# Kernel optimization log

Measured on AMD Instinct MI355X. Metric: run time of the kernel, lower is better.

## Reference

```python
import jax, jax.numpy as jnp
import numpy as np

TEMPERATURE = 0.2
EPS = 1e-10

def setup_inputs() -> dict:
    key = jax.random.key(0)
    x = jax.random.normal(key, (8, 1024, 64, 64), dtype=jnp.float32)
    return {"x": x}

def reference(x):
    B, C, H, W = x.shape
    xf = x.reshape(B, C, H * W)                      # [B, C, HW]
    dot = jnp.einsum('bcn,bdn->bcd', xf, xf) / TEMPERATURE  # [B, C, C]
    logits = jax.nn.softmax(dot, axis=-1)
    diag = jnp.diagonal(logits, axis1=-2, axis2=-1)  # [B, C]
    loss = -jnp.log(diag + EPS)
    return jnp.mean(loss)
```

## Files before the change

kernel.cpp:

```cpp
#include <hip/hip_runtime.h>
#include <hip/hip_bf16.h>

#define BATCH 8
#define CCH 1024
#define NHW 4096
#define SCALE 5.0f
#define ROWS (BATCH * CCH)
#define NTILES 72
#define NTICK (BATCH * NTILES)
#define GRID_G 512

typedef unsigned char u8;
typedef unsigned int u32;
typedef __attribute__((ext_vector_type(4))) float float4v;
typedef __attribute__((ext_vector_type(4))) u32 uint4v;

__device__ __forceinline__ void async_load16(const void* gsrc, void* ldst) {
    __builtin_amdgcn_global_load_lds(
        (__attribute__((address_space(1))) void*)gsrc,
        (__attribute__((address_space(3))) void*)ldst,
        16, 0, 0);
}

__device__ __forceinline__ u32 pk4_fp8(float a, float b, float c, float d) {
    u32 v = __builtin_amdgcn_cvt_pk_fp8_f32(a, b, 0, false);
    v = __builtin_amdgcn_cvt_pk_fp8_f32(c, d, v, true);
    return v;
}

__device__ __forceinline__ float ssq4_fp8(u32 q) {
    float d0 = __builtin_amdgcn_cvt_f32_fp8(q, 0);
    float d1 = __builtin_amdgcn_cvt_f32_fp8(q, 1);
    float d2 = __builtin_amdgcn_cvt_f32_fp8(q, 2);
    float d3 = __builtin_amdgcn_cvt_f32_fp8(q, 3);
    return d0 * d0 + d1 * d1 + d2 * d2 + d3 * d3;
}

template <bool CONVERT>
__global__ __launch_bounds__(256) void prep_kernel(const float* __restrict__ x,
                                                   u8* __restrict__ xq,
                                                   float* __restrict__ diag,
                                                   float* __restrict__ l_acc,
                                                   int* __restrict__ counters) {
    const int row = blockIdx.x;
    const int tid = threadIdx.x;
    const float* src = x + (size_t)row * NHW;
    float ssum = 0.f;
#pragma unroll
    for (int p = 0; p < 4; ++p) {
        const int idx = p * 1024 + tid * 4;
        float4 v = *(const float4*)(src + idx);
        const u32 q = pk4_fp8(v.x, v.y, v.z, v.w);
        ssum += ssq4_fp8(q);
        if (CONVERT) *(u32*)(xq + (size_t)row * NHW + idx) = q;
    }
#pragma unroll
    for (int m = 1; m < 64; m <<= 1) ssum += __shfl_xor(ssum, m);
    __shared__ float red[4];
    if ((tid & 63) == 0) red[tid >> 6] = ssum;
    __syncthreads();
    if (tid == 0) {
        diag[row] = (red[0] + red[1] + red[2] + red[3]) * SCALE;
        l_acc[row] = 0.f;
        if (row == 0) { counters[0] = 0; counters[1] = 0; }
    }
}

template <bool QSRC>
__global__ __launch_bounds__(256) void gram_kernel(const u8* __restrict__ Xq,
                                                   const float* __restrict__ Xf,
                                                   const float* __restrict__ diag,
                                                   float* __restrict__ l_acc,
                                                   float* __restrict__ num,
                                                   int* __restrict__ counters,
                                                   float* __restrict__ out) {
    __shared__ __align__(16) u8 As[2][16384];
    __shared__ __align__(16) u8 Bs[2][8192];
    __shared__ int s_ticket;
    __shared__ float s_red[4];

    const int tid  = threadIdx.x;
    const int lane = tid & 63;
    const int w    = tid >> 6;
    const int wm   = w >> 1;
    const int wn   = w & 1;

    const int st_r  = lane >> 3;
    const int st_kc = (lane & 7) ^ st_r;

    const int q_  = lane >> 4;
    const int cl  = lane & 15;

    for (;;) {
        if (tid == 0) s_ticket = atomicAdd(counters + 0, 1);
        __syncthreads();
        const int tk = s_ticket;
        if (tk >= NTICK) break;

        const int b = tk & 7;
        const int t = tk >> 3;
        int bi = 0;
#pragma unroll
        for (int i = 7; i >= 1; --i) {
            if (t >= i * (17 - i)) { bi = i; break; }
        }
        const int bj2 = 2 * bi + (t - bi * (17 - bi));
        const bool aliasB = (bj2 == 2 * bi) || (bj2 == 2 * bi + 1);

        const u8*    pA  = nullptr; const u8*    pB  = nullptr;
        const float* pAf = nullptr; const float* pBf = nullptr;
        if (QSRC) {
            const u8* baseX = Xq + (size_t)b * CCH * NHW;
            pA = baseX + (size_t)(bi * 128 + w * 32 + st_r) * NHW + st_kc * 16;
            pB = baseX + (size_t)(bj2 * 64 + w * 16 + st_r) * NHW + st_kc * 16;
        } else {
            const float* baseXf = Xf + (size_t)b * CCH * NHW;
            pAf = baseXf + (size_t)(bi * 128 + w * 32 + st_r) * NHW + st_kc * 16;
            pBf = baseXf + (size_t)(bj2 * 64 + w * 16 + st_r) * NHW + st_kc * 16;
        }

        auto stage = [&](int buf, int K0) {
            if (QSRC) {
#pragma unroll
                for (int t8 = 0; t8 < 4; ++t8)
                    async_load16(pA + (size_t)(t8 * 8) * NHW + K0,
                                 As[buf] + (size_t)(w * 32 + t8 * 8) * 128);
                if (!aliasB) {
#pragma unroll
                    for (int t8 = 0; t8 < 2; ++t8)
                        async_load16(pB + (size_t)(t8 * 8) * NHW + K0,
                                     Bs[buf] + (size_t)(w * 16 + t8 * 8) * 128);
                }
            } else {
#pragma unroll
                for (int t8 = 0; t8 < 4; ++t8) {
                    const float* s = pAf + (size_t)(t8 * 8) * NHW + K0;
                    float4 f0 = *(const float4*)(s);
                    float4 f1 = *(const float4*)(s + 4);
                    float4 f2 = *(const float4*)(s + 8);
                    float4 f3 = *(const float4*)(s + 12);
                    uint4v d;
                    d.x = pk4_fp8(f0.x, f0.y, f0.z, f0.w);
                    d.y = pk4_fp8(f1.x, f1.y, f1.z, f1.w);
                    d.z = pk4_fp8(f2.x, f2.y, f2.z, f2.w);
                    d.w = pk4_fp8(f3.x, f3.y, f3.z, f3.w);
                    *(uint4v*)(As[buf] + (size_t)(w * 32 + t8 * 8 + st_r) * 128 + (lane & 7) * 16) = d;
                }
                if (!aliasB) {
#pragma unroll
                    for (int t8 = 0; t8 < 2; ++t8) {
                        const float* s = pBf + (size_t)(t8 * 8) * NHW + K0;
                        float4 f0 = *(const float4*)(s);
                        float4 f1 = *(const float4*)(s + 4);
                        float4 f2 = *(const float4*)(s + 8);
                        float4 f3 = *(const float4*)(s + 12);
                        uint4v d;
                        d.x = pk4_fp8(f0.x, f0.y, f0.z, f0.w);
                        d.y = pk4_fp8(f1.x, f1.y, f1.z, f1.w);
                        d.z = pk4_fp8(f2.x, f2.y, f2.z, f2.w);
                        d.w = pk4_fp8(f3.x, f3.y, f3.z, f3.w);
                        *(uint4v*)(Bs[buf] + (size_t)(w * 16 + t8 * 8 + st_r) * 128 + (lane & 7) * 16) = d;
                    }
                }
            }
        };

        float4v acc[4][2] = {};

        stage(0, 0);
        __syncthreads();

        for (int i = 0; i < NHW / 128; ++i) {
            const int cur = i & 1;
            const int K0n = (i + 1) * 128;
            if (K0n < NHW) stage(cur ^ 1, K0n);

            const u8* Ab = As[cur];
            const u8* Bb = aliasB ? (Ab + (size_t)(bj2 - 2 * bi) * 64 * 128) : Bs[cur];
            const int rl = lane & 15;
#pragma unroll
            for (int s = 0; s < 4; ++s) {
                const int cbase = 2 * s + (q_ >> 1);
                const int boff  = (int)((cbase ^ (rl & 7)) * 16 + (q_ & 1) * 8);
                long af[4], bf[2];
#pragma unroll
                for (int mt = 0; mt < 4; ++mt)
                    af[mt] = *(const long*)(Ab + (size_t)(wm * 64 + mt * 16 + rl) * 128 + boff);
#pragma unroll
                for (int nt = 0; nt < 2; ++nt)
                    bf[nt] = *(const long*)(Bb + (size_t)(wn * 32 + nt * 16 + rl) * 128 + boff);
#pragma unroll
                for (int mt = 0; mt < 4; ++mt)
#pragma unroll
                    for (int nt = 0; nt < 2; ++nt)
                        acc[mt][nt] = __builtin_amdgcn_mfma_f32_16x16x32_fp8_fp8(af[mt], bf[nt], acc[mt][nt], 0, 0, 0);
            }
            __syncthreads();
        }

        const int rowbase = bi * 128 + wm * 64;
        const int colbase = bj2 * 64 + wn * 32;
        const float* dgb = diag + b * CCH;
        float* lb = l_acc + b * CCH;

#pragma unroll
        for (int mt = 0; mt < 4; ++mt) {
#pragma unroll
            for (int reg = 0; reg < 4; ++reg) {
                const int gr = rowbase + mt * 16 + q_ * 4 + reg;
                const float dg = dgb[gr];
                float s = 0.f;
#pragma unroll
                for (int nt = 0; nt < 2; ++nt) {
                    const int gc = colbase + nt * 16 + cl;
                    const float e = __expf(acc[mt][nt][reg] * SCALE - dg);
                    if (gr <= gc) s += e;
                    if (gr == gc) num[b * CCH + gr] = e;
                }
                s += __shfl_xor(s, 1);
                s += __shfl_xor(s, 2);
                s += __shfl_xor(s, 4);
                s += __shfl_xor(s, 8);
                if (cl == 0) atomicAdd(lb + gr, s);
            }
        }

#pragma unroll
        for (int nt = 0; nt < 2; ++nt) {
            const int gc = colbase + nt * 16 + cl;
            const float dgc = dgb[gc];
            float s = 0.f;
#pragma unroll
            for (int mt = 0; mt < 4; ++mt) {
#pragma unroll
                for (int reg = 0; reg < 4; ++reg) {
                    const int gr = rowbase + mt * 16 + q_ * 4 + reg;
                    if (gr < gc) s += __expf(acc[mt][nt][reg] * SCALE - dgc);
                }
            }
            s += __shfl_xor(s, 16);
            s += __shfl_xor(s, 32);
            if (lane < 16) atomicAdd(lb + gc, s);
        }
    }

    __syncthreads();
    if (tid == 0) {
        __threadfence();
        const int old = atomicAdd(counters + 1, 1);
        s_ticket = (old == GRID_G - 1) ? 1 : 0;
    }
    __syncthreads();
    if (s_ticket) {
        __threadfence();
        float s = 0.f;
        for (int r = tid; r < ROWS; r += 256) {
            const float d = num[r] / l_acc[r];
            s += -__logf(d + 1e-10f);
        }
#pragma unroll
        for (int m = 1; m < 64; m <<= 1) s += __shfl_xor(s, m);
        if ((tid & 63) == 0) s_red[tid >> 6] = s;
        __syncthreads();
        if (tid == 0)
            out[0] = (s_red[0] + s_red[1] + s_red[2] + s_red[3]) * (1.0f / (float)ROWS);
    }
}

extern "C" void kernel_launch(void* const* d_in, const int* in_sizes, int n_in,
                              void* d_out, int out_size, void* d_ws, size_t ws_size,
                              hipStream_t stream) {
    const float* x = (const float*)d_in[0];
    float* out = (float*)d_out;

    const size_t xq_bytes   = (size_t)BATCH * CCH * NHW;
    const size_t stat_bytes = (size_t)ROWS * 4;
    const bool fast = ws_size >= xq_bytes + 3 * stat_bytes + 64;

    if (fast) {
        u8*    xq    = (u8*)d_ws;
        float* diag  = (float*)((char*)d_ws + xq_bytes);
        float* l_acc = diag + ROWS;
        float* num   = l_acc + ROWS;
        int*   cnt   = (int*)(num + ROWS);
        prep_kernel<true><<<ROWS, 256, 0, stream>>>(x, xq, diag, l_acc, cnt);
        gram_kernel<true><<<GRID_G, 256, 0, stream>>>(xq, nullptr, diag, l_acc, num, cnt, out);
    } else {
        float* diag  = (float*)d_ws;
        float* l_acc = diag + ROWS;
        float* num   = l_acc + ROWS;
        int*   cnt   = (int*)(num + ROWS);
        prep_kernel<false><<<ROWS, 256, 0, stream>>>(x, nullptr, diag, l_acc, cnt);
        gram_kernel<false><<<GRID_G, 256, 0, stream>>>(nullptr, x, diag, l_acc, num, cnt, out);
    }
}
```

Measured before the change: 295.2 us.

## Permute fp8 K layout for 128-bit LDS reads and drop persistent ticket loop

The prep kernel now writes the fp8 copy of x with a permuted K ordering inside each 128-byte span, so each lane can fetch two MFMA k-slices with one 16-byte LDS read instead of two 8-byte reads. The fallback float path applies the same permutation when converting on the fly. The persistent atomic-ticket work loop is replaced with a static one-tile-per-block grid of 576 blocks, which removes the per-tile atomic and barrier at the cost of dynamic load balancing. The grid size change depends on the launch code, which is not visible.

New measurement: 249.3 us. -15.6%, faster.

```diff
diff --git a/kernel.cpp b/kernel.cpp
--- a/kernel.cpp
+++ b/kernel.cpp
@@ -7,13 +7,12 @@
 #define SCALE 5.0f
 #define ROWS (BATCH * CCH)
 #define NTILES 72
-#define NTICK (BATCH * NTILES)
-#define GRID_G 512
+#define GRID_G (BATCH * NTILES)
 
 typedef unsigned char u8;
 typedef unsigned int u32;
 typedef __attribute__((ext_vector_type(4))) float float4v;
-typedef __attribute__((ext_vector_type(4))) u32 uint4v;
+typedef __attribute__((ext_vector_type(2))) long long2v;
 
 __device__ __forceinline__ void async_load16(const void* gsrc, void* ldst) {
     __builtin_amdgcn_global_load_lds(
@@ -34,6 +33,10 @@
     float d2 = __builtin_amdgcn_cvt_f32_fp8(q, 2);
     float d3 = __builtin_amdgcn_cvt_f32_fp8(q, 3);
     return d0 * d0 + d1 * d1 + d2 * d2 + d3 * d3;
+}
+
+__device__ __forceinline__ int kperm(int L) {
+    return ((L >> 3) << 3) + ((L & 3) << 1) + ((L >> 2) & 1);
 }
 
 template <bool CONVERT>
@@ -52,7 +55,13 @@
         float4 v = *(const float4*)(src + idx);
         const u32 q = pk4_fp8(v.x, v.y, v.z, v.w);
         ssum += ssq4_fp8(q);
-        if (CONVERT) *(u32*)(xq + (size_t)row * NHW + idx) = q;
+        if (CONVERT) {
+            const int span = idx >> 7;
+            const int kin  = idx & 127;
+            const int P    = kperm(kin >> 3);
+            const int sub  = kin & 7;
+            *(u32*)(xq + (size_t)row * NHW + span * 128 + P * 8 + sub) = q;
+        }
     }
 #pragma unroll
     for (int m = 1; m < 64; m <<= 1) ssum += __shfl_xor(ssum, m);
@@ -62,7 +71,7 @@
     if (tid == 0) {
         diag[row] = (red[0] + red[1] + red[2] + red[3]) * SCALE;
         l_acc[row] = 0.f;
-        if (row == 0) { counters[0] = 0; counters[1] = 0; }
+        if (row == 0) counters[0] = 0;
     }
 }
 
@@ -76,8 +85,20 @@
                                                    float* __restrict__ out) {
     __shared__ __align__(16) u8 As[2][16384];
     __shared__ __align__(16) u8 Bs[2][8192];
-    __shared__ int s_ticket;
+    __shared__ int s_flag;
     __shared__ float s_red[4];
+
+    const int bid = blockIdx.x;
+    const int b = bid & 7;
+    const int t = bid >> 3;
+
+    int bi = 0;
+#pragma unroll
+    for (int i = 7; i >= 1; --i) {
+        if (t >= i * (17 - i)) { bi = i; break; }
+    }
+    const int bj2 = 2 * bi + (t - bi * (17 - bi));
+    const bool aliasB = (bj2 == 2 * bi) || (bj2 == 2 * bi + 1);
 
     const int tid  = threadIdx.x;
     const int lane = tid & 63;
@@ -89,169 +110,153 @@
     const int st_kc = (lane & 7) ^ st_r;
 
     const int q_  = lane >> 4;
-    const int cl  = lane & 15;
-
-    for (;;) {
-        if (tid == 0) s_ticket = atomicAdd(counters + 0, 1);
-        __syncthreads();
-        const int tk = s_ticket;
-        if (tk >= NTICK) break;
-
-        const int b = tk & 7;
-        const int t = tk >> 3;
-        int bi = 0;
-#pragma unroll
-        for (int i = 7; i >= 1; --i) {
-            if (t >= i * (17 - i)) { bi = i; break; }
-        }
-        const int bj2 = 2 * bi + (t - bi * (17 - bi));
-        const bool aliasB = (bj2 == 2 * bi) || (bj2 == 2 * bi + 1);
-
-        const u8*    pA  = nullptr; const u8*    pB  = nullptr;
-        const float* pAf = nullptr; const float* pBf = nullptr;
+    const int rl  = lane & 15;
+
+    const u8*    pA  = nullptr; const u8*    pB  = nullptr;
+    const float* pAf = nullptr; const float* pBf = nullptr;
+    if (QSRC) {
+        const u8* baseX = Xq + (size_t)b * CCH * NHW;
+        pA = baseX + (size_t)(bi * 128 + w * 32 + st_r) * NHW + st_kc * 16;
+        pB = baseX + (size_t)(bj2 * 64 + w * 16 + st_r) * NHW + st_kc * 16;
+    } else {
+        const float* baseXf = Xf + (size_t)b * CCH * NHW;
+        pAf = baseXf + (size_t)(bi * 128 + w * 32 + st_r) * NHW;
+        pBf = baseXf + (size_t)(bj2 * 64 + w * 16 + st_r) * NHW;
+    }
+
+    auto stage = [&](int buf, int K0) {
         if (QSRC) {
-            const u8* baseX = Xq + (size_t)b * CCH * NHW;
-            pA = baseX + (size_t)(bi * 128 + w * 32 + st_r) * NHW + st_kc * 16;
-            pB = baseX + (size_t)(bj2 * 64 + w * 16 + st_r) * NHW + st_kc * 16;
+#pragma unroll
+            for (int t8 = 0; t8 < 4; ++t8)
+                async_load16(pA + (size_t)(t8 * 8) * NHW + K0,
+                             As[buf] + (size_t)(w * 32 + t8 * 8) * 128);
+            if (!aliasB) {
+#pragma unroll
+                for (int t8 = 0; t8 < 2; ++t8)
+                    async_load16(pB + (size_t)(t8 * 8) * NHW + K0,
+                                 Bs[buf] + (size_t)(w * 16 + t8 * 8) * 128);
+            }
         } else {
-            const float* baseXf = Xf + (size_t)b * CCH * NHW;
-            pAf = baseXf + (size_t)(bi * 128 + w * 32 + st_r) * NHW + st_kc * 16;
-            pBf = baseXf + (size_t)(bj2 * 64 + w * 16 + st_r) * NHW + st_kc * 16;
-        }
-
-        auto stage = [&](int buf, int K0) {
-            if (QSRC) {
-#pragma unroll
-                for (int t8 = 0; t8 < 4; ++t8)
-                    async_load16(pA + (size_t)(t8 * 8) * NHW + K0,
-                                 As[buf] + (size_t)(w * 32 + t8 * 8) * 128);
-                if (!aliasB) {
-#pragma unroll
-                    for (int t8 = 0; t8 < 2; ++t8)
-                        async_load16(pB + (size_t)(t8 * 8) * NHW + K0,
-                                     Bs[buf] + (size_t)(w * 16 + t8 * 8) * 128);
-                }
-            } else {
-#pragma unroll
-                for (int t8 = 0; t8 < 4; ++t8) {
-                    const float* s = pAf + (size_t)(t8 * 8) * NHW + K0;
+#pragma unroll
+            for (int t8 = 0; t8 < 4; ++t8) {
+                u8* drow = As[buf] + (size_t)(w * 32 + t8 * 8 + st_r) * 128 + (lane & 7) * 16;
+#pragma unroll
+                for (int h = 0; h < 2; ++h) {
+                    const int p = 2 * st_kc + h;
+                    const int L = ((p >> 3) << 3) + ((p & 1) << 2) + ((p & 7) >> 1);
+                    const float* s = pAf + (size_t)(t8 * 8) * NHW + K0 + L * 8;
                     float4 f0 = *(const float4*)(s);
                     float4 f1 = *(const float4*)(s + 4);
-                    float4 f2 = *(const float4*)(s + 8);
-                    float4 f3 = *(const float4*)(s + 12);
-                    uint4v d;
-                    d.x = pk4_fp8(f0.x, f0.y, f0.z, f0.w);
-                    d.y = pk4_fp8(f1.x, f1.y, f1.z, f1.w);
-                    d.z = pk4_fp8(f2.x, f2.y, f2.z, f2.w);
-                    d.w = pk4_fp8(f3.x, f3.y, f3.z, f3.w);
-                    *(uint4v*)(As[buf] + (size_t)(w * 32 + t8 * 8 + st_r) * 128 + (lane & 7) * 16) = d;
+                    ((u32*)(drow + h * 8))[0] = pk4_fp8(f0.x, f0.y, f0.z, f0.w);
+                    ((u32*)(drow + h * 8))[1] = pk4_fp8(f1.x, f1.y, f1.z, f1.w);
                 }
-                if (!aliasB) {
-#pragma unroll
-                    for (int t8 = 0; t8 < 2; ++t8) {
-                        const float* s = pBf + (size_t)(t8 * 8) * NHW + K0;
+            }
+            if (!aliasB) {
+#pragma unroll
+                for (int t8 = 0; t8 < 2; ++t8) {
+                    u8* drow = Bs[buf] + (size_t)(w * 16 + t8 * 8 + st_r) * 128 + (lane & 7) * 16;
+#pragma unroll
+                    for (int h = 0; h < 2; ++h) {
+                        const int p = 2 * st_kc + h;
+                        const int L = ((p >> 3) << 3) + ((p & 1) << 2) + ((p & 7) >> 1);
+                        const float* s = pBf + (size_t)(t8 * 8) * NHW + K0 + L * 8;
                         float4 f0 = *(const float4*)(s);
                         float4 f1 = *(const float4*)(s + 4);
-                        float4 f2 = *(const float4*)(s + 8);
-                        float4 f3 = *(const float4*)(s + 12);
-                        uint4v d;
-                        d.x = pk4_fp8(f0.x, f0.y, f0.z, f0.w);
-                        d.y = pk4_fp8(f1.x, f1.y, f1.z, f1.w);
-                        d.z = pk4_fp8(f2.x, f2.y, f2.z, f2.w);
-                        d.w = pk4_fp8(f3.x, f3.y, f3.z, f3.w);
-                        *(uint4v*)(Bs[buf] + (size_t)(w * 16 + t8 * 8 + st_r) * 128 + (lane & 7) * 16) = d;
+                        ((u32*)(drow + h * 8))[0] = pk4_fp8(f0.x, f0.y, f0.z, f0.w);
+                        ((u32*)(drow + h * 8))[1] = pk4_fp8(f1.x, f1.y, f1.z, f1.w);
                     }
                 }
             }
-        };
-
-        float4v acc[4][2] = {};
-
-        stage(0, 0);
+        }
+    };
+
+    float4v acc[4][2] = {};
+
+    stage(0, 0);
+    __syncthreads();
+
+    for (int i = 0; i < NHW / 128; ++i) {
+        const int cur = i & 1;
+        const int K0n = (i + 1) * 128;
+        if (K0n < NHW) stage(cur ^ 1, K0n);
+
+        const u8* Ab = As[cur];
+        const u8* Bb = aliasB ? (Ab + (size_t)(bj2 - 2 * bi) * 64 * 128) : Bs[cur];
+#pragma unroll
+        for (int sp = 0; sp < 2; ++sp) {
+            const int boff = ((sp * 4 + q_) ^ (rl & 7)) * 16;
+            long2v a2[4], b2[2];
+#pragma unroll
+            for (int mt = 0; mt < 4; ++mt)
+                a2[mt] = *(const long2v*)(Ab + (size_t)(wm * 64 + mt * 16 + rl) * 128 + boff);
+#pragma unroll
+            for (int nt = 0; nt < 2; ++nt)
+                b2[nt] = *(const long2v*)(Bb + (size_t)(wn * 32 + nt * 16 + rl) * 128 + boff);
+#pragma unroll
+            for (int mt = 0; mt < 4; ++mt)
+#pragma unroll
+                for (int nt = 0; nt < 2; ++nt) {
+                    acc[mt][nt] = __builtin_amdgcn_mfma_f32_16x16x32_fp8_fp8(a2[mt].x, b2[nt].x, acc[mt][nt], 0, 0, 0);
+                    acc[mt][nt] = __builtin_amdgcn_mfma_f32_16x16x32_fp8_fp8(a2[mt].y, b2[nt].y, acc[mt][nt], 0, 0, 0);
+                }
+        }
         __syncthreads();
-
-        for (int i = 0; i < NHW / 128; ++i) {
-            const int cur = i & 1;
-            const int K0n = (i + 1) * 128;
-            if (K0n < NHW) stage(cur ^ 1, K0n);
-
-            const u8* Ab = As[cur];
-            const u8* Bb = aliasB ? (Ab + (size_t)(bj2 - 2 * bi) * 64 * 128) : Bs[cur];
-            const int rl = lane & 15;
-#pragma unroll
-            for (int s = 0; s < 4; ++s) {
-                const int cbase = 2 * s + (q_ >> 1);
-                const int boff  = (int)((cbase ^ (rl & 7)) * 16 + (q_ & 1) * 8);
-                long af[4], bf[2];
-#pragma unroll
-                for (int mt = 0; mt < 4; ++mt)
-                    af[mt] = *(const long*)(Ab + (size_t)(wm * 64 + mt * 16 + rl) * 128 + boff);
-#pragma unroll
-                for (int nt = 0; nt < 2; ++nt)
-                    bf[nt] = *(const long*)(Bb + (size_t)(wn * 32 + nt * 16 + rl) * 128 + boff);
-#pragma unroll
-                for (int mt = 0; mt < 4; ++mt)
-#pragma unroll
-                    for (int nt = 0; nt < 2; ++nt)
-                        acc[mt][nt] = __builtin_amdgcn_mfma_f32_16x16x32_fp8_fp8(af[mt], bf[nt], acc[mt][nt], 0, 0, 0);
-            }
-            __syncthreads();
-        }
-
-        const int rowbase = bi * 128 + wm * 64;
-        const int colbase = bj2 * 64 + wn * 32;
-        const float* dgb = diag + b * CCH;
-        float* lb = l_acc + b * CCH;
-
+    }
+
+    const int cl = rl;
+    const int rowbase = bi * 128 + wm * 64;
+    const int colbase = bj2 * 64 + wn * 32;
+    const float* dgb = diag + b * CCH;
+    float* lb = l_acc + b * CCH;
+
+#pragma unroll
+    for (int mt = 0; mt < 4; ++mt) {
+#pragma unroll
+        for (int reg = 0; reg < 4; ++reg) {
+            const int gr = rowbase + mt * 16 + q_ * 4 + reg;
+            const float dg = dgb[gr];
+            float s = 0.f;
+#pragma unroll
+            for (int nt = 0; nt < 2; ++nt) {
+                const int gc = colbase + nt * 16 + cl;
+                const float e = __expf(acc[mt][nt][reg] * SCALE - dg);
+                if (gr <= gc) s += e;
+                if (gr == gc) num[b * CCH + gr] = e;
+            }
+            s += __shfl_xor(s, 1);
+            s += __shfl_xor(s, 2);
+            s += __shfl_xor(s, 4);
+            s += __shfl_xor(s, 8);
+            if (cl == 0) atomicAdd(lb + gr, s);
+        }
+    }
+
+#pragma unroll
+    for (int nt = 0; nt < 2; ++nt) {
+        const int gc = colbase + nt * 16 + cl;
+        const float dgc = dgb[gc];
+        float s = 0.f;
 #pragma unroll
         for (int mt = 0; mt < 4; ++mt) {
 #pragma unroll
             for (int reg = 0; reg < 4; ++reg) {
                 const int gr = rowbase + mt * 16 + q_ * 4 + reg;
-                const float dg = dgb[gr];
-                float s = 0.f;
-#pragma unroll
-                for (int nt = 0; nt < 2; ++nt) {
-                    const int gc = colbase + nt * 16 + cl;
-                    const float e = __expf(acc[mt][nt][reg] * SCALE - dg);
-                    if (gr <= gc) s += e;
-                    if (gr == gc) num[b * CCH + gr] = e;
-                }
-                s += __shfl_xor(s, 1);
-                s += __shfl_xor(s, 2);
-                s += __shfl_xor(s, 4);
-                s += __shfl_xor(s, 8);
-                if (cl == 0) atomicAdd(lb + gr, s);
-            }
-        }
-
-#pragma unroll
-        for (int nt = 0; nt < 2; ++nt) {
-            const int gc = colbase + nt * 16 + cl;
-            const float dgc = dgb[gc];
-            float s = 0.f;
-#pragma unroll
-            for (int mt = 0; mt < 4; ++mt) {
-#pragma unroll
-                for (int reg = 0; reg < 4; ++reg) {
-                    const int gr = rowbase + mt * 16 + q_ * 4 + reg;
-                    if (gr < gc) s += __expf(acc[mt][nt][reg] * SCALE - dgc);
-                }
-            }
-            s += __shfl_xor(s, 16);
-            s += __shfl_xor(s, 32);
-            if (lane < 16) atomicAdd(lb + gc, s);
-        }
+                if (gr < gc) s += __expf(acc[mt][nt][reg] * SCALE - dgc);
+            }
+        }
+        s += __shfl_xor(s, 16);
+        s += __shfl_xor(s, 32);
+        if (lane < 16) atomicAdd(lb + gc, s);
     }
 
     __syncthreads();
     if (tid == 0) {
         __threadfence();
-        const int old = atomicAdd(counters + 1, 1);
-        s_ticket = (old == GRID_G - 1) ? 1 : 0;
+        const int old = atomicAdd(counters + 0, 1);
+        s_flag = (old == GRID_G - 1) ? 1 : 0;
     }
     __syncthreads();
-    if (s_ticket) {
+    if (s_flag) {
         __threadfence();
         float s = 0.f;
         for (int r = tid; r < ROWS; r += 256) {
```

## Replace persistent atomic work queue with one-block-per-tile static grid

Applied to the files above, without the earlier changes.

Drops the persistent-kernel ticket loop, where 512 blocks fetched tiles through an atomic counter. Instead one block is launched per tile (576) and the tile is derived from blockIdx, which removes the per-tile atomic and barrier and lets the hardware scheduler balance blocks. The last-block final reduction is also unrolled with four independent accumulators to give more memory-level parallelism. The launch-site grid size is not visible here and must match the new GRID_G, and a 576-block grid may leave a partial tail wave.

After: 247.7 us. 1.19x faster.

```diff
diff --git a/kernel.cpp b/kernel.cpp
--- a/kernel.cpp
+++ b/kernel.cpp
@@ -7,8 +7,7 @@
 #define SCALE 5.0f
 #define ROWS (BATCH * CCH)
 #define NTILES 72
-#define NTICK (BATCH * NTILES)
-#define GRID_G 512
+#define GRID_G (BATCH * NTILES)
 
 typedef unsigned char u8;
 typedef unsigned int u32;
@@ -62,7 +61,7 @@
     if (tid == 0) {
         diag[row] = (red[0] + red[1] + red[2] + red[3]) * SCALE;
         l_acc[row] = 0.f;
-        if (row == 0) { counters[0] = 0; counters[1] = 0; }
+        if (row == 0) counters[0] = 0;
     }
 }
 
@@ -76,8 +75,20 @@
                                                    float* __restrict__ out) {
     __shared__ __align__(16) u8 As[2][16384];
     __shared__ __align__(16) u8 Bs[2][8192];
-    __shared__ int s_ticket;
+    __shared__ int s_flag;
     __shared__ float s_red[4];
+
+    const int bid = blockIdx.x;
+    const int b = bid & 7;
+    const int t = bid >> 3;
+
+    int bi = 0;
+#pragma unroll
+    for (int i = 7; i >= 1; --i) {
+        if (t >= i * (17 - i)) { bi = i; break; }
+    }
+    const int bj2 = 2 * bi + (t - bi * (17 - bi));
+    const bool aliasB = (bj2 == 2 * bi) || (bj2 == 2 * bi + 1);
 
     const int tid  = threadIdx.x;
     const int lane = tid & 63;
@@ -88,53 +99,49 @@
     const int st_r  = lane >> 3;
     const int st_kc = (lane & 7) ^ st_r;
 
-    const int q_  = lane >> 4;
-    const int cl  = lane & 15;
-
-    for (;;) {
-        if (tid == 0) s_ticket = atomicAdd(counters + 0, 1);
-        __syncthreads();
-        const int tk = s_ticket;
-        if (tk >= NTICK) break;
-
-        const int b = tk & 7;
-        const int t = tk >> 3;
-        int bi = 0;
-#pragma unroll
-        for (int i = 7; i >= 1; --i) {
-            if (t >= i * (17 - i)) { bi = i; break; }
-        }
-        const int bj2 = 2 * bi + (t - bi * (17 - bi));
-        const bool aliasB = (bj2 == 2 * bi) || (bj2 == 2 * bi + 1);
-
-        const u8*    pA  = nullptr; const u8*    pB  = nullptr;
-        const float* pAf = nullptr; const float* pBf = nullptr;
+    const u8*    pA  = nullptr; const u8*    pB  = nullptr;
+    const float* pAf = nullptr; const float* pBf = nullptr;
+    if (QSRC) {
+        const u8* baseX = Xq + (size_t)b * CCH * NHW;
+        pA = baseX + (size_t)(bi * 128 + w * 32 + st_r) * NHW + st_kc * 16;
+        pB = baseX + (size_t)(bj2 * 64 + w * 16 + st_r) * NHW + st_kc * 16;
+    } else {
+        const float* baseXf = Xf + (size_t)b * CCH * NHW;
+        pAf = baseXf + (size_t)(bi * 128 + w * 32 + st_r) * NHW + st_kc * 16;
+        pBf = baseXf + (size_t)(bj2 * 64 + w * 16 + st_r) * NHW + st_kc * 16;
+    }
+
+    auto stage = [&](int buf, int K0) {
         if (QSRC) {
-            const u8* baseX = Xq + (size_t)b * CCH * NHW;
-            pA = baseX + (size_t)(bi * 128 + w * 32 + st_r) * NHW + st_kc * 16;
-            pB = baseX + (size_t)(bj2 * 64 + w * 16 + st_r) * NHW + st_kc * 16;
+#pragma unroll
+            for (int t8 = 0; t8 < 4; ++t8)
+                async_load16(pA + (size_t)(t8 * 8) * NHW + K0,
+                             As[buf] + (size_t)(w * 32 + t8 * 8) * 128);
+            if (!aliasB) {
+#pragma unroll
+                for (int t8 = 0; t8 < 2; ++t8)
+                    async_load16(pB + (size_t)(t8 * 8) * NHW + K0,
+                                 Bs[buf] + (size_t)(w * 16 + t8 * 8) * 128);
+            }
         } else {
-            const float* baseXf = Xf + (size_t)b * CCH * NHW;
-            pAf = baseXf + (size_t)(bi * 128 + w * 32 + st_r) * NHW + st_kc * 16;
-            pBf = baseXf + (size_t)(bj2 * 64 + w * 16 + st_r) * NHW + st_kc * 16;
-        }
-
-        auto stage = [&](int buf, int K0) {
-            if (QSRC) {
-#pragma unroll
-                for (int t8 = 0; t8 < 4; ++t8)
-                    async_load16(pA + (size_t)(t8 * 8) * NHW + K0,
-                                 As[buf] + (size_t)(w * 32 + t8 * 8) * 128);
-                if (!aliasB) {
-#pragma unroll
-                    for (int t8 = 0; t8 < 2; ++t8)
-                        async_load16(pB + (size_t)(t8 * 8) * NHW + K0,
-                                     Bs[buf] + (size_t)(w * 16 + t8 * 8) * 128);
-                }
-            } else {
-#pragma unroll
-                for (int t8 = 0; t8 < 4; ++t8) {
-                    const float* s = pAf + (size_t)(t8 * 8) * NHW + K0;
+#pragma unroll
+            for (int t8 = 0; t8 < 4; ++t8) {
+                const float* s = pAf + (size_t)(t8 * 8) * NHW + K0;
+                float4 f0 = *(const float4*)(s);
+                float4 f1 = *(const float4*)(s + 4);
+                float4 f2 = *(const float4*)(s + 8);
+                float4 f3 = *(const float4*)(s + 12);
+                uint4v d;
+                d.x = pk4_fp8(f0.x, f0.y, f0.z, f0.w);
+                d.y = pk4_fp8(f1.x, f1.y, f1.z, f1.w);
+                d.z = pk4_fp8(f2.x, f2.y, f2.z, f2.w);
+                d.w = pk4_fp8(f3.x, f3.y, f3.z, f3.w);
+                *(uint4v*)(As[buf] + (size_t)(w * 32 + t8 * 8 + st_r) * 128 + (lane & 7) * 16) = d;
+            }
+            if (!aliasB) {
+#pragma unroll
+                for (int t8 = 0; t8 < 2; ++t8) {
+                    const float* s = pBf + (size_t)(t8 * 8) * NHW + K0;
                     float4 f0 = *(const float4*)(s);
                     float4 f1 = *(const float4*)(s + 4);
                     float4 f2 = *(const float4*)(s + 8);
@@ -144,120 +151,155 @@
                     d.y = pk4_fp8(f1.x, f1.y, f1.z, f1.w);
                     d.z = pk4_fp8(f2.x, f2.y, f2.z, f2.w);
                     d.w = pk4_fp8(f3.x, f3.y, f3.z, f3.w);
-                    *(uint4v*)(As[buf] + (size_t)(w * 32 + t8 * 8 + st_r) * 128 + (lane & 7) * 16) = d;
+                    *(uint4v*)(Bs[buf] + (size_t)(w * 16 + t8 * 8 + st_r) * 128 + (lane & 7) * 16) = d;
                 }
-                if (!aliasB) {
-#pragma unroll
-                    for (int t8 = 0; t8 < 2; ++t8) {
-                        const float* s = pBf + (size_t)(t8 * 8) * NHW + K0;
-                        float4 f0 = *(const float4*)(s);
-                        float4 f1 = *(const float4*)(s + 4);
-                        float4 f2 = *(const float4*)(s + 8);
-                        float4 f3 = *(const float4*)(s + 12);
-                        uint4v d;
-                        d.x = pk4_fp8(f0.x, f0.y, f0.z, f0.w);
-                        d.y = pk4_fp8(f1.x, f1.y, f1.z, f1.w);
-                        d.z = pk4_fp8(f2.x, f2.y, f2.z, f2.w);
-                        d.w = pk4_fp8(f3.x, f3.y, f3.z, f3.w);
-                        *(uint4v*)(Bs[buf] + (size_t)(w * 16 + t8 * 8 + st_r) * 128 + (lane & 7) * 16) = d;
-                    }
-                }
-            }
-        };
-
-        float4v acc[4][2] = {};
-
-        stage(0, 0);
+            }
+        }
+    };
+
+    float4v acc[4][2] = {};
+
+    stage(0, 0);
+    __syncthreads();
+
+    for (int i = 0; i < NHW / 128; ++i) {
+        const int cur = i & 1;
+        const int K0n = (i + 1) * 128;
+        if (K0n < NHW) stage(cur ^ 1, K0n);
+
+        const u8* Ab = As[cur];
+        const u8* Bb = aliasB ? (Ab + (size_t)(bj2 - 2 * bi) * 64 * 128) : Bs[cur];
+        const int q  = lane >> 4;
+        const int rl = lane & 15;
+#pragma unroll
+        for (int s = 0; s < 4; ++s) {
+            const int cbase = 2 * s + (q >> 1);
+            const int boff  = (int)((cbase ^ (rl & 7)) * 16 + (q & 1) * 8);
+            long af[4], bf[2];
+#pragma unroll
+            for (int mt = 0; mt < 4; ++mt)
+                af[mt] = *(const long*)(Ab + (size_t)(wm * 64 + mt * 16 + rl) * 128 + boff);
+#pragma unroll
+            for (int nt = 0; nt < 2; ++nt)
+                bf[nt] = *(const long*)(Bb + (size_t)(wn * 32 + nt * 16 + rl) * 128 + boff);
+#pragma unroll
+            for (int mt = 0; mt < 4; ++mt)
+#pragma unroll
+                for (int nt = 0; nt < 2; ++nt)
+                    acc[mt][nt] = __builtin_amdgcn_mfma_f32_16x16x32_fp8_fp8(af[mt], bf[nt], acc[mt][nt], 0, 0, 0);
+        }
         __syncthreads();
-
-        for (int i = 0; i < NHW / 128; ++i) {
-            const int cur = i & 1;
-            const int K0n = (i + 1) * 128;
-            if (K0n < NHW) stage(cur ^ 1, K0n);
-
-            const u8* Ab = As[cur];
-            const u8* Bb = aliasB ? (Ab + (size_t)(bj2 - 2 * bi) * 64 * 128) : Bs[cur];
-            const int rl = lane & 15;
-#pragma unroll
-            for (int s = 0; s < 4; ++s) {
-                const int cbase = 2 * s + (q_ >> 1);
-                const int boff  = (int)((cbase ^ (rl & 7)) * 16 + (q_ & 1) * 8);
-                long af[4], bf[2];
-#pragma unroll
-                for (int mt = 0; mt < 4; ++mt)
-                    af[mt] = *(const long*)(Ab + (size_t)(wm * 64 + mt * 16 + rl) * 128 + boff);
-#pragma unroll
-                for (int nt = 0; nt < 2; ++nt)
-                    bf[nt] = *(const long*)(Bb + (size_t)(wn * 32 + nt * 16 + rl) * 128 + boff);
-#pragma unroll
-                for (int mt = 0; mt < 4; ++mt)
-#pragma unroll
-                    for (int nt = 0; nt < 2; ++nt)
-                        acc[mt][nt] = __builtin_amdgcn_mfma_f32_16x16x32_fp8_fp8(af[mt], bf[nt], acc[mt][nt], 0, 0, 0);
-            }
-            __syncthreads();
-        }
-
-        const int rowbase = bi * 128 + wm * 64;
-        const int colbase = bj2 * 64 + wn * 32;
-        const float* dgb = diag + b * CCH;
-        float* lb = l_acc + b * CCH;
-
+    }
+
+    const int q_  = lane >> 4;
+    const int cl  = lane & 15;
+    const int rowbase = bi * 128 + wm * 64;
+    const int colbase = bj2 * 64 + wn * 32;
+    const float* dgb = diag + b * CCH;
+    float* lb = l_acc + b * CCH;
+
+#pragma unroll
+    for (int mt = 0; mt < 4; ++mt) {
+#pragma unroll
+        for (int reg = 0; reg < 4; ++reg) {
+            const int gr = rowbase + mt * 16 + q_ * 4 + reg;
+            const float dg = dgb[gr];
+            float s = 0.f;
+#pragma unroll
+            for (int nt = 0; nt < 2; ++nt) {
+                const int gc = colbase + nt * 16 + cl;
+                const float e = __expf(acc[mt][nt][reg] * SCALE - dg);
+                if (gr <= gc) s += e;
+                if (gr == gc) num[b * CCH + gr] = e;
+            }
+            s += __shfl_xor(s, 1);
+            s += __shfl_xor(s, 2);
+            s += __shfl_xor(s, 4);
+            s += __shfl_xor(s, 8);
+            if (cl == 0) atomicAdd(lb + gr, s);
+        }
+    }
+
+#pragma unroll
+    for (int nt = 0; nt < 2; ++nt) {
+        const int gc = colbase + nt * 16 + cl;
+        const float dgc = dgb[gc];
+        float s = 0.f;
 #pragma unroll
         for (int mt = 0; mt < 4; ++mt) {
 #pragma unroll
             for (int reg = 0; reg < 4; ++reg) {
                 const int gr = rowbase + mt * 16 + q_ * 4 + reg;
-                const float dg = dgb[gr];
-                float s = 0.f;
-#pragma unroll
-                for (int nt = 0; nt < 2; ++nt) {
-                    const int gc = colbase + nt * 16 + cl;
-                    const float e = __expf(acc[mt][nt][reg] * SCALE - dg);
-                    if (gr <= gc) s += e;
-                    if (gr == gc) num[b * CCH + gr] = e;
-                }
-                s += __shfl_xor(s, 1);
-                s += __shfl_xor(s, 2);
-                s += __shfl_xor(s, 4);
-                s += __shfl_xor(s, 8);
-                if (cl == 0) atomicAdd(lb + gr, s);
-            }
-        }
-
-#pragma unroll
-        for (int nt = 0; nt < 2; ++nt) {
-            const int gc = colbase + nt * 16 + cl;
-            const float dgc = dgb[gc];
-            float s = 0.f;
-#pragma unroll
-            for (int mt = 0; mt < 4; ++mt) {
-#pragma unroll
-                for (int reg = 0; reg < 4; ++reg) {
-                    const int gr = rowbase + mt * 16 + q_ * 4 + reg;
-                    if (gr < gc) s += __expf(acc[mt][nt][reg] * SCALE - dgc);
-                }
-            }
-            s += __shfl_xor(s, 16);
-            s += __shfl_xor(s, 32);
-            if (lane < 16) atomicAdd(lb + gc, s);
-        }
+                if (gr < gc) s += __expf(acc[mt][nt][reg] * SCALE - dgc);
+            }
+        }
+        s += __shfl_xor(s, 16);
+        s += __shfl_xor(s, 32);
+        if (lane < 16) atomicAdd(lb + gc, s);
     }
 
     __syncthreads();
     if (tid == 0) {
         __threadfence();
-        const int old = atomicAdd(counters + 1, 1);
-        s_ticket = (old == GRID_G - 1) ? 1 : 0;
+        const int old = atomicAdd(counters + 0, 1);
+        s_flag = (old == GRID_G - 1) ? 1 : 0;
     }
     __syncthreads();
-    if (s_ticket) {
+    if (s_flag) {
         __threadfence();
-        float s = 0.f;
-        for (int r = tid; r < ROWS; r += 256) {
-            const float d = num[r] / l_acc[r];
-            s += -__logf(d + 1e-10f);
-        }
+        float s0 = 0.f, s1 = 0.f, s2 = 0.f, s3 = 0.f;
+#pragma unroll
+        for (int ib = 0; ib < 8; ib += 4) {
+            const int r0 = (ib + 0) * 1024 + tid;
+            const int r1 = (ib + 1) * 1024 + tid;
+            const int r2 = (ib + 2) * 1024 + tid;
+            const int r3 = (ib + 3) * 1024 + tid;
+            const float d0 = num[r0] / l_acc[r0];
+            const float d1 = num[r1] / l_acc[r1];
+            const float d2 = num[r2] / l_acc[r2];
+            const float d3 = num[r3] / l_acc[r3];
+            s0 += -__logf(d0 + 1e-10f);
+            s1 += -__logf(d1 + 1e-10f);
+            s2 += -__logf(d2 + 1e-10f);
+            s3 += -__logf(d3 + 1e-10f);
+            const int r4 = (ib + 0) * 1024 + 256 + tid;
+            const int r5 = (ib + 1) * 1024 + 256 + tid;
+            const int r6 = (ib + 2) * 1024 + 256 + tid;
+            const int r7 = (ib + 3) * 1024 + 256 + tid;
+            const float d4 = num[r4] / l_acc[r4];
+            const float d5 = num[r5] / l_acc[r5];
+            const float d6 = num[r6] / l_acc[r6];
+            const float d7 = num[r7] / l_acc[r7];
+            s0 += -__logf(d4 + 1e-10f);
+            s1 += -__logf(d5 + 1e-10f);
+            s2 += -__logf(d6 + 1e-10f);
+            s3 += -__logf(d7 + 1e-10f);
+            const int r8 = (ib + 0) * 1024 + 512 + tid;
+            const int r9 = (ib + 1) * 1024 + 512 + tid;
+            const int rA = (ib + 2) * 1024 + 512 + tid;
+            const int rB = (ib + 3) * 1024 + 512 + tid;
+            const float d8 = num[r8] / l_acc[r8];
+            const float d9 = num[r9] / l_acc[r9];
+            const float dA = num[rA] / l_acc[rA];
+            const float dB = num[rB] / l_acc[rB];
+            s0 += -__logf(d8 + 1e-10f);
+            s1 += -__logf(d9 + 1e-10f);
+            s2 += -__logf(dA + 1e-10f);
+            s3 += -__logf(dB + 1e-10f);
+            const int rC = (ib + 0) * 1024 + 768 + tid;
+            const int rD = (ib + 1) * 1024 + 768 + tid;
+            const int rE = (ib + 2) * 1024 + 768 + tid;
+            const int rF = (ib + 3) * 1024 + 768 + tid;
+            const float dC = num[rC] / l_acc[rC];
+            const float dD = num[rD] / l_acc[rD];
+            const float dE = num[rE] / l_acc[rE];
+            const float dF = num[rF] / l_acc[rF];
+            s0 += -__logf(dC + 1e-10f);
+            s1 += -__logf(dD + 1e-10f);
+            s2 += -__logf(dE + 1e-10f);
+            s3 += -__logf(dF + 1e-10f);
+        }
+        float s = (s0 + s1) + (s2 + s3);
 #pragma unroll
         for (int m = 1; m < 64; m <<= 1) s += __shfl_xor(s, m);
         if ((tid & 63) == 0) s_red[tid >> 6] = s;
```
